# Performance work log

Hardware: AMD Instinct MI355X
Metric: run time of the kernel (lower is better)

## Reference

```python
import jax, jax.numpy as jnp
import numpy as np


def setup_inputs() -> dict:
    key = jax.random.key(0)
    k1, k2 = jax.random.split(key)
    B, M, QT, KVT, H = 4, 16, 1024, 1024, 64
    s = jax.random.normal(k1, (B, M, QT, KVT), dtype=jnp.float32)
    v = jax.random.normal(k2, (B, M, KVT, H), dtype=jnp.float32)
    return {"s": s, "v": v}


def reference(s, v):
    # Original: broadcast-multiply [B,M,QT,KVT,H] then sum over KVT.
    # Mathematically a batched matmul: out[b,m,q,h] = sum_k s[b,m,q,k] * v[b,m,k,h]
    return jnp.einsum('bmqk,bmkh->bmqh', s, v)
```

## Files before the change

kernel.cpp:

```cpp
#include <hip/hip_runtime.h>
#include <stdint.h>


typedef __bf16 bf16x8 __attribute__((ext_vector_type(8)));
typedef float  f32x4  __attribute__((ext_vector_type(4)));

#define QTDIM 1024
#define KVDIM 1024
#define HDIM  64
#define QTILE 64
#define BK    64
#define NK    (KVDIM / BK)
#define SSTR  72
#define THREADS 256

__device__ __forceinline__ uint32_t pack_bf16_2(float lo, float hi) {
    union { float f; uint32_t u; } a, b;
    a.f = lo; b.f = hi;
    return __builtin_amdgcn_perm(b.u, a.u, 0x07060302u);
}

__global__ __launch_bounds__(THREADS, 4) void svbmm_kernel(
    const float* __restrict__ s, const float* __restrict__ v, float* __restrict__ out)
{
    __shared__ uint16_t s_sm[2][QTILE * SSTR];
    __shared__ uint16_t vt_sm[2][HDIM * SSTR];

    const int tid = threadIdx.x;
    const int bm  = blockIdx.y;
    const int q0  = blockIdx.x * QTILE;

    const float* sp = s   + ((size_t)bm * QTDIM + q0) * (size_t)KVDIM;
    const float* vp = v   + (size_t)bm * KVDIM * HDIM;
    float*       op = out + ((size_t)bm * QTDIM + q0) * (size_t)HDIM;

    const int srow = tid >> 4;
    const int scol = (tid & 15) << 2;
    const int vh   = tid & 63;
    const int vk0  = (tid >> 6) << 4;

    float4 sreg[4];
    float  vreg[16];

    {
        const float* sb = sp + srow * KVDIM + scol;
        #pragma unroll
        for (int i = 0; i < 4; ++i)
            sreg[i] = *(const float4*)(sb + i * 16 * KVDIM);
        const float* vb = vp + vk0 * HDIM + vh;
        #pragma unroll
        for (int j = 0; j < 16; ++j)
            vreg[j] = vb[j * HDIM];
    }

    f32x4 acc[4];
    #pragma unroll
    for (int nt = 0; nt < 4; ++nt)
        acc[nt] = (f32x4){0.f, 0.f, 0.f, 0.f};

    const int wave = tid >> 6;
    const int lane = tid & 63;
    const int lrow = lane & 15;
    const int quad = lane >> 4;

    #pragma unroll 2
    for (int kt = 0; kt < NK; ++kt) {
        const int buf = kt & 1;

        #pragma unroll
        for (int i = 0; i < 4; ++i) {
            float4 f = sreg[i];
            uint64_t u = (uint64_t)pack_bf16_2(f.x, f.y)
                       | ((uint64_t)pack_bf16_2(f.z, f.w) << 32);
            *(uint64_t*)&s_sm[buf][(srow + i * 16) * SSTR + scol] = u;
        }
        #pragma unroll
        for (int p = 0; p < 4; ++p) {
            uint64_t u = (uint64_t)pack_bf16_2(vreg[4 * p],     vreg[4 * p + 1])
                       | ((uint64_t)pack_bf16_2(vreg[4 * p + 2], vreg[4 * p + 3]) << 32);
            *(uint64_t*)&vt_sm[buf][vh * SSTR + vk0 + 4 * p] = u;
        }

        __syncthreads();

        if (kt + 1 < NK) {
            const float* sb = sp + srow * KVDIM + (kt + 1) * BK + scol;
            #pragma unroll
            for (int i = 0; i < 4; ++i)
                sreg[i] = *(const float4*)(sb + i * 16 * KVDIM);
            const float* vb = vp + ((kt + 1) * BK + vk0) * HDIM + vh;
            #pragma unroll
            for (int j = 0; j < 16; ++j)
                vreg[j] = vb[j * HDIM];
        }

        #pragma unroll
        for (int kk = 0; kk < 2; ++kk) {
            const int col = kk * 32 + quad * 8;
            bf16x8 a = *(const bf16x8*)&s_sm[buf][(wave * 16 + lrow) * SSTR + col];
            #pragma unroll
            for (int nt = 0; nt < 4; ++nt) {
                bf16x8 b = *(const bf16x8*)&vt_sm[buf][(nt * 16 + lrow) * SSTR + col];
                acc[nt] = __builtin_amdgcn_mfma_f32_16x16x32_bf16(a, b, acc[nt], 0, 0, 0);
            }
        }
    }

    #pragma unroll
    for (int nt = 0; nt < 4; ++nt) {
        #pragma unroll
        for (int r = 0; r < 4; ++r) {
            const int row = wave * 16 + quad * 4 + r;
            const int col = nt * 16 + lrow;
            op[row * HDIM + col] = acc[nt][r];
        }
    }
}

extern "C" void kernel_launch(void* const* d_in, const int* in_sizes, int n_in,
                              void* d_out, int out_size, void* d_ws, size_t ws_size,
                              hipStream_t stream) {
    const float* s = (const float*)d_in[0];
    const float* v = (const float*)d_in[1];
    float* out = (float*)d_out;
    const int BM = in_sizes[0] / (QTDIM * KVDIM);
    dim3 grid(QTDIM / QTILE, BM);
    svbmm_kernel<<<grid, THREADS, 0, stream>>>(s, v, out);
}
```

Measured before the change: 381.6 us.

## Load S fragments directly into registers and swap grid axes

The A operand (S) no longer goes through LDS. Each lane loads its MFMA fragment straight from global memory as float4s, converts it to bf16 in registers, and feeds it to the MFMA. This removes the LDS stores and reads for S and halves LDS usage. The grid is also transposed so that consecutive blocks walk over batch-heads rather than query tiles, which changes L2 reuse of V and the order of memory traffic. The trade-off is that global loads for S are now less coalesced: each row is split into 32-byte chunks per lane.

```diff
diff --git a/kernel.cpp b/kernel.cpp
--- a/kernel.cpp
+++ b/kernel.cpp
@@ -4,6 +4,7 @@
 
 typedef __bf16 bf16x8 __attribute__((ext_vector_type(8)));
 typedef float  f32x4  __attribute__((ext_vector_type(4)));
+typedef uint32_t u32x4 __attribute__((ext_vector_type(4)));
 
 #define QTDIM 1024
 #define KVDIM 1024
@@ -23,34 +24,37 @@
 __global__ __launch_bounds__(THREADS, 4) void svbmm_kernel(
     const float* __restrict__ s, const float* __restrict__ v, float* __restrict__ out)
 {
-    __shared__ uint16_t s_sm[2][QTILE * SSTR];
     __shared__ uint16_t vt_sm[2][HDIM * SSTR];
 
     const int tid = threadIdx.x;
-    const int bm  = blockIdx.y;
-    const int q0  = blockIdx.x * QTILE;
+    const int bm  = blockIdx.x;
+    const int q0  = blockIdx.y * QTILE;
 
     const float* sp = s   + ((size_t)bm * QTDIM + q0) * (size_t)KVDIM;
     const float* vp = v   + (size_t)bm * KVDIM * HDIM;
     float*       op = out + ((size_t)bm * QTDIM + q0) * (size_t)HDIM;
 
-    const int srow = tid >> 4;
-    const int scol = (tid & 15) << 2;
-    const int vh   = tid & 63;
-    const int vk0  = (tid >> 6) << 4;
+    const int wave = tid >> 6;
+    const int lane = tid & 63;
+    const int lrow = lane & 15;
+    const int quad = lane >> 4;
 
-    float4 sreg[4];
+    const float* ap = sp + (wave * 16 + lrow) * KVDIM + quad * 8;
+
+    const int vh  = tid & 63;
+    const int vk0 = (tid >> 6) << 4;
+
+    float4 a4[4];
     float  vreg[16];
 
     {
-        const float* sb = sp + srow * KVDIM + scol;
-        #pragma unroll
-        for (int i = 0; i < 4; ++i)
-            sreg[i] = *(const float4*)(sb + i * 16 * KVDIM);
         const float* vb = vp + vk0 * HDIM + vh;
         #pragma unroll
         for (int j = 0; j < 16; ++j)
             vreg[j] = vb[j * HDIM];
+        #pragma unroll
+        for (int i = 0; i < 4; ++i)
+            a4[i] = *(const float4*)(ap + (i >> 1) * 32 + (i & 1) * 4);
     }
 
     f32x4 acc[4];
@@ -58,22 +62,10 @@
     for (int nt = 0; nt < 4; ++nt)
         acc[nt] = (f32x4){0.f, 0.f, 0.f, 0.f};
 
-    const int wave = tid >> 6;
-    const int lane = tid & 63;
-    const int lrow = lane & 15;
-    const int quad = lane >> 4;
-
     #pragma unroll 2
     for (int kt = 0; kt < NK; ++kt) {
         const int buf = kt & 1;
 
-        #pragma unroll
-        for (int i = 0; i < 4; ++i) {
-            float4 f = sreg[i];
-            uint64_t u = (uint64_t)pack_bf16_2(f.x, f.y)
-                       | ((uint64_t)pack_bf16_2(f.z, f.w) << 32);
-            *(uint64_t*)&s_sm[buf][(srow + i * 16) * SSTR + scol] = u;
-        }
         #pragma unroll
         for (int p = 0; p < 4; ++p) {
             uint64_t u = (uint64_t)pack_bf16_2(vreg[4 * p],     vreg[4 * p + 1])
@@ -83,25 +75,36 @@
 
         __syncthreads();
 
+        bf16x8 afrag[2];
+        #pragma unroll
+        for (int kk = 0; kk < 2; ++kk) {
+            union { u32x4 u; bf16x8 b; } fa;
+            float4 lo = a4[kk * 2], hi = a4[kk * 2 + 1];
+            fa.u[0] = pack_bf16_2(lo.x, lo.y);
+            fa.u[1] = pack_bf16_2(lo.z, lo.w);
+            fa.u[2] = pack_bf16_2(hi.x, hi.y);
+            fa.u[3] = pack_bf16_2(hi.z, hi.w);
+            afrag[kk] = fa.b;
+        }
+
         if (kt + 1 < NK) {
-            const float* sb = sp + srow * KVDIM + (kt + 1) * BK + scol;
-            #pragma unroll
-            for (int i = 0; i < 4; ++i)
-                sreg[i] = *(const float4*)(sb + i * 16 * KVDIM);
             const float* vb = vp + ((kt + 1) * BK + vk0) * HDIM + vh;
             #pragma unroll
             for (int j = 0; j < 16; ++j)
                 vreg[j] = vb[j * HDIM];
+            const float* ab = ap + (kt + 1) * BK;
+            #pragma unroll
+            for (int i = 0; i < 4; ++i)
+                a4[i] = *(const float4*)(ab + (i >> 1) * 32 + (i & 1) * 4);
         }
 
         #pragma unroll
         for (int kk = 0; kk < 2; ++kk) {
             const int col = kk * 32 + quad * 8;
-            bf16x8 a = *(const bf16x8*)&s_sm[buf][(wave * 16 + lrow) * SSTR + col];
             #pragma unroll
             for (int nt = 0; nt < 4; ++nt) {
                 bf16x8 b = *(const bf16x8*)&vt_sm[buf][(nt * 16 + lrow) * SSTR + col];
-                acc[nt] = __builtin_amdgcn_mfma_f32_16x16x32_bf16(a, b, acc[nt], 0, 0, 0);
+                acc[nt] = __builtin_amdgcn_mfma_f32_16x16x32_bf16(afrag[kk], b, acc[nt], 0, 0, 0);
             }
         }
     }
@@ -124,6 +127,6 @@
     const float* v = (const float*)d_in[1];
     float* out = (float*)d_out;
     const int BM = in_sizes[0] / (QTDIM * KVDIM);
-    dim3 grid(QTDIM / QTILE, BM);
+    dim3 grid(BM, QTDIM / QTILE);
     svbmm_kernel<<<grid, THREADS, 0, stream>>>(s, v, out);
 }
```

Result: no change. 386.4 us (+1.3%).

## Prefetch two K-tiles ahead with dual register sets and swap grid block order

Applied to the files above, without the earlier changes.

Global loads are now issued two K-tiles ahead using two alternating register sets, with the loop manually unrolled by two, so more memory latency is hidden behind MFMA work. __syncthreads is replaced by an inline-asm lgkmcnt wait plus s_barrier, which does not wait on outstanding global loads. The grid is transposed so that consecutive blocks cover different batch-head slices rather than adjacent q tiles of the same slice, which changes how work is spread and how the shared V data is reused across the cache. The cost is roughly double the prefetch register footprint, which may reduce occupancy under the launch bound. The lighter barrier also assumes no outstanding LDS hazards.

```diff
diff --git a/kernel.cpp b/kernel.cpp
--- a/kernel.cpp
+++ b/kernel.cpp
@@ -20,6 +20,10 @@
     return __builtin_amdgcn_perm(b.u, a.u, 0x07060302u);
 }
 
+__device__ __forceinline__ void lds_barrier() {
+    asm volatile("s_waitcnt lgkmcnt(0)\n\ts_barrier" ::: "memory");
+}
+
 __global__ __launch_bounds__(THREADS, 4) void svbmm_kernel(
     const float* __restrict__ s, const float* __restrict__ v, float* __restrict__ out)
 {
@@ -27,8 +31,8 @@
     __shared__ uint16_t vt_sm[2][HDIM * SSTR];
 
     const int tid = threadIdx.x;
-    const int bm  = blockIdx.y;
-    const int q0  = blockIdx.x * QTILE;
+    const int bm  = blockIdx.x;
+    const int q0  = blockIdx.y * QTILE;
 
     const float* sp = s   + ((size_t)bm * QTDIM + q0) * (size_t)KVDIM;
     const float* vp = v   + (size_t)bm * KVDIM * HDIM;
@@ -39,72 +43,76 @@
     const int vh   = tid & 63;
     const int vk0  = (tid >> 6) << 4;
 
-    float4 sreg[4];
-    float  vreg[16];
-
-    {
-        const float* sb = sp + srow * KVDIM + scol;
-        #pragma unroll
-        for (int i = 0; i < 4; ++i)
-            sreg[i] = *(const float4*)(sb + i * 16 * KVDIM);
-        const float* vb = vp + vk0 * HDIM + vh;
-        #pragma unroll
-        for (int j = 0; j < 16; ++j)
-            vreg[j] = vb[j * HDIM];
-    }
-
-    f32x4 acc[4];
-    #pragma unroll
-    for (int nt = 0; nt < 4; ++nt)
-        acc[nt] = (f32x4){0.f, 0.f, 0.f, 0.f};
-
     const int wave = tid >> 6;
     const int lane = tid & 63;
     const int lrow = lane & 15;
     const int quad = lane >> 4;
 
-    #pragma unroll 2
-    for (int kt = 0; kt < NK; ++kt) {
-        const int buf = kt & 1;
+    float4 sregA[4], sregB[4];
+    float  vregA[16], vregB[16];
 
+    {
+        const float* sb = sp + srow * KVDIM + scol;
+        const float* vb = vp + vk0 * HDIM + vh;
         #pragma unroll
-        for (int i = 0; i < 4; ++i) {
-            float4 f = sreg[i];
-            uint64_t u = (uint64_t)pack_bf16_2(f.x, f.y)
-                       | ((uint64_t)pack_bf16_2(f.z, f.w) << 32);
-            *(uint64_t*)&s_sm[buf][(srow + i * 16) * SSTR + scol] = u;
-        }
+        for (int i = 0; i < 4; ++i) sregA[i] = *(const float4*)(sb + i * 16 * KVDIM);
         #pragma unroll
-        for (int p = 0; p < 4; ++p) {
-            uint64_t u = (uint64_t)pack_bf16_2(vreg[4 * p],     vreg[4 * p + 1])
-                       | ((uint64_t)pack_bf16_2(vreg[4 * p + 2], vreg[4 * p + 3]) << 32);
-            *(uint64_t*)&vt_sm[buf][vh * SSTR + vk0 + 4 * p] = u;
-        }
+        for (int j = 0; j < 16; ++j) vregA[j] = vb[j * HDIM];
+        sb += BK; vb += BK * HDIM;
+        #pragma unroll
+        for (int i = 0; i < 4; ++i) sregB[i] = *(const float4*)(sb + i * 16 * KVDIM);
+        #pragma unroll
+        for (int j = 0; j < 16; ++j) vregB[j] = vb[j * HDIM];
+    }
 
-        __syncthreads();
+    f32x4 acc[4];
+    #pragma unroll
+    for (int nt = 0; nt < 4; ++nt) acc[nt] = (f32x4){0.f, 0.f, 0.f, 0.f};
 
-        if (kt + 1 < NK) {
-            const float* sb = sp + srow * KVDIM + (kt + 1) * BK + scol;
-            #pragma unroll
-            for (int i = 0; i < 4; ++i)
-                sreg[i] = *(const float4*)(sb + i * 16 * KVDIM);
-            const float* vb = vp + ((kt + 1) * BK + vk0) * HDIM + vh;
-            #pragma unroll
-            for (int j = 0; j < 16; ++j)
-                vreg[j] = vb[j * HDIM];
-        }
+#define BODY(KT, BUF, SR, VR)                                                   \
+    do {                                                                        \
+        _Pragma("unroll")                                                       \
+        for (int i = 0; i < 4; ++i) {                                           \
+            float4 f = SR[i];                                                   \
+            uint64_t u = (uint64_t)pack_bf16_2(f.x, f.y)                        \
+                       | ((uint64_t)pack_bf16_2(f.z, f.w) << 32);               \
+            *(uint64_t*)&s_sm[BUF][(srow + i * 16) * SSTR + scol] = u;          \
+        }                                                                       \
+        _Pragma("unroll")                                                       \
+        for (int p = 0; p < 4; ++p) {                                           \
+            uint64_t u = (uint64_t)pack_bf16_2(VR[4 * p],     VR[4 * p + 1])    \
+                       | ((uint64_t)pack_bf16_2(VR[4 * p + 2], VR[4 * p + 3]) << 32); \
+            *(uint64_t*)&vt_sm[BUF][vh * SSTR + vk0 + 4 * p] = u;               \
+        }                                                                       \
+        lds_barrier();                                                          \
+        if ((KT) + 2 < NK) {                                                    \
+            const float* sb2 = sp + srow * KVDIM + ((KT) + 2) * BK + scol;      \
+            _Pragma("unroll")                                                   \
+            for (int i = 0; i < 4; ++i)                                         \
+                SR[i] = *(const float4*)(sb2 + i * 16 * KVDIM);                 \
+            const float* vb2 = vp + (((KT) + 2) * BK + vk0) * HDIM + vh;        \
+            _Pragma("unroll")                                                   \
+            for (int j = 0; j < 16; ++j)                                        \
+                VR[j] = vb2[j * HDIM];                                          \
+        }                                                                       \
+        _Pragma("unroll")                                                       \
+        for (int kk = 0; kk < 2; ++kk) {                                        \
+            const int col = kk * 32 + quad * 8;                                 \
+            bf16x8 a = *(const bf16x8*)&s_sm[BUF][(wave * 16 + lrow) * SSTR + col]; \
+            _Pragma("unroll")                                                   \
+            for (int nt = 0; nt < 4; ++nt) {                                    \
+                bf16x8 b = *(const bf16x8*)&vt_sm[BUF][(nt * 16 + lrow) * SSTR + col]; \
+                acc[nt] = __builtin_amdgcn_mfma_f32_16x16x32_bf16(a, b, acc[nt], 0, 0, 0); \
+            }                                                                   \
+        }                                                                       \
+    } while (0)
 
-        #pragma unroll
-        for (int kk = 0; kk < 2; ++kk) {
-            const int col = kk * 32 + quad * 8;
-            bf16x8 a = *(const bf16x8*)&s_sm[buf][(wave * 16 + lrow) * SSTR + col];
-            #pragma unroll
-            for (int nt = 0; nt < 4; ++nt) {
-                bf16x8 b = *(const bf16x8*)&vt_sm[buf][(nt * 16 + lrow) * SSTR + col];
-                acc[nt] = __builtin_amdgcn_mfma_f32_16x16x32_bf16(a, b, acc[nt], 0, 0, 0);
-            }
-        }
+    #pragma unroll 1
+    for (int kt = 0; kt < NK; kt += 2) {
+        BODY(kt,     0, sregA, vregA);
+        BODY(kt + 1, 1, sregB, vregB);
     }
+#undef BODY
 
     #pragma unroll
     for (int nt = 0; nt < 4; ++nt) {
@@ -124,6 +132,6 @@
     const float* v = (const float*)d_in[1];
     float* out = (float*)d_out;
     const int BM = in_sizes[0] / (QTDIM * KVDIM);
-    dim3 grid(QTDIM / QTILE, BM);
+    dim3 grid(BM, QTDIM / QTILE);
     svbmm_kernel<<<grid, THREADS, 0, stream>>>(s, v, out);
 }
```

Measured after the change: 383.2 us. Within noise of the previous version (+0.4%).
